# Kernel tuning notes

Measured on AMD Instinct MI355X. Metric: run time of the kernel, lower is better.

## Reference

```python
import jax, jax.numpy as jnp
import numpy as np

C_IN = 256
C_KEY = 128
C_VAL = 256


def setup_inputs() -> dict:
    key = jax.random.key(0)
    ks = jax.random.split(key, 10)
    B, H, W = 8, 64, 64
    s_in = 1.0 / np.sqrt(C_IN)
    s_val = 1.0 / np.sqrt(C_VAL)
    return {
        "x": jax.random.normal(ks[0], (B, C_IN, H, W), jnp.float32),
        "Wk": jax.random.uniform(ks[1], (C_KEY, C_IN), jnp.float32, -s_in, s_in),
        "bk": jax.random.uniform(ks[2], (C_KEY,), jnp.float32, -s_in, s_in),
        "Wq": jax.random.uniform(ks[3], (C_KEY, C_IN), jnp.float32, -s_in, s_in),
        "bq": jax.random.uniform(ks[4], (C_KEY,), jnp.float32, -s_in, s_in),
        "Wv": jax.random.uniform(ks[5], (C_VAL, C_IN), jnp.float32, -s_in, s_in),
        "bv": jax.random.uniform(ks[6], (C_VAL,), jnp.float32, -s_in, s_in),
        "Wr": jax.random.uniform(ks[7], (C_IN, C_VAL), jnp.float32, -s_val, s_val),
        "br": jax.random.uniform(ks[8], (C_IN,), jnp.float32, -s_val, s_val),
        "gamma": jnp.zeros((1,), jnp.float32) + 0.5,  # nonzero so attention path is exercised
    }


def reference(x, Wk, bk, Wq, bq, Wv, bv, Wr, br, gamma):
    B, C, H, W = x.shape
    N = H * W
    xf = x.reshape(B, C, N)  # [B, C, N]
    # 1x1 convs == per-pixel linear projections
    k = jnp.einsum('kc,bcn->bkn', Wk, xf) + bk[None, :, None]   # [B, Ck, N]
    q = jnp.einsum('kc,bcn->bkn', Wq, xf) + bq[None, :, None]   # [B, Ck, N]
    v = jnp.einsum('vc,bcn->bvn', Wv, xf) + bv[None, :, None]   # [B, Cv, N]
    # attention = q^T k, softmax over keys (no scaling, per original)
    att = jnp.einsum('bkq,bkn->bqn', q, k)                      # [B, N, N]
    att = jax.nn.softmax(att, axis=-1)
    out = jnp.einsum('bvn,bqn->bvq', v, att)                    # [B, Cv, N]
    out = jnp.einsum('cv,bvn->bcn', Wr, out) + br[None, :, None]
    out = out.reshape(B, C, H, W)
    return gamma * out + x
```

## Files before the change

### kernel.cpp

```cpp
#include <hip/hip_runtime.h>
#include <hip/hip_bf16.h>
#include <stdint.h>

#define NPIX 4096

typedef __attribute__((ext_vector_type(8))) short bf16x8;
typedef __attribute__((ext_vector_type(16))) float f32x16;
typedef __attribute__((ext_vector_type(4))) unsigned int uint4v;

__device__ __forceinline__ unsigned short bfb(float f) {
  __hip_bfloat16 h = __float2bfloat16(f);
  return __builtin_bit_cast(unsigned short, h);
}
__device__ __forceinline__ unsigned pack2(float a, float b) {
  return (unsigned)bfb(a) | ((unsigned)bfb(b) << 16);
}
__device__ __forceinline__ f32x16 mfma32(bf16x8 a, bf16x8 b, f32x16 c) {
  return __builtin_amdgcn_mfma_f32_32x32x16_bf16(a, b, c, 0, 0, 0);
}

__global__ void k_cvt(const float* __restrict__ Wq, const float* __restrict__ Wk,
                      const float* __restrict__ Wv, const float* __restrict__ Wr,
                      unsigned short* __restrict__ wqk, unsigned short* __restrict__ wv,
                      unsigned short* __restrict__ wr) {
  int i = blockIdx.x * 256 + threadIdx.x;
  wqk[i] = bfb(i < 32768 ? Wq[i] : Wk[i - 32768]);
  wv[i]  = bfb(Wv[i]);
  wr[i]  = bfb(Wr[i]);
}

__launch_bounds__(256, 2)
__global__ void k_qkv(const float* __restrict__ x,
                      const unsigned short* __restrict__ wqk,
                      const unsigned short* __restrict__ wv,
                      const float* __restrict__ bq, const float* __restrict__ bk,
                      const float* __restrict__ bv,
                      unsigned short* __restrict__ qT, unsigned short* __restrict__ kT,
                      unsigned short* __restrict__ vV) {
  __shared__ __align__(16) unsigned short xT[64 * 256];
  const int b = blockIdx.x & 7;
  const int n0 = (blockIdx.x >> 3) * 64;
  const int t = threadIdx.x;
  const float* xb = x + (size_t)b * 256 * NPIX;
  #pragma unroll
  for (int p = 0; p < 16; ++p) {
    int c = (t >> 4) + p * 16;
    int nq = (t & 15) * 4;
    float4 f = *reinterpret_cast<const float4*>(xb + (size_t)c * NPIX + n0 + nq);
    float vals[4] = {f.x, f.y, f.z, f.w};
    #pragma unroll
    for (int j = 0; j < 4; ++j) {
      int n = nq + j;
      int byteoff = n * 512 + ((c * 2) ^ ((n & 7) << 4));
      xT[byteoff >> 1] = bfb(vals[j]);
    }
  }
  __syncthreads();
  const int lane = t & 63, w = t >> 6, l31 = lane & 31, hi = lane >> 5;
  f32x16 aq[2][2], av[2][2];
  #pragma unroll
  for (int a0 = 0; a0 < 2; ++a0)
    #pragma unroll
    for (int a1 = 0; a1 < 2; ++a1)
      #pragma unroll
      for (int i = 0; i < 16; ++i) { aq[a0][a1][i] = 0.f; av[a0][a1][i] = 0.f; }
  #pragma unroll
  for (int s = 0; s < 16; ++s) {
    bf16x8 xa[2];
    #pragma unroll
    for (int nt = 0; nt < 2; ++nt) {
      int n = nt * 32 + l31;
      int byteoff = n * 512 + (((s * 32 + hi * 16)) ^ ((n & 7) << 4));
      xa[nt] = *reinterpret_cast<const bf16x8*>(reinterpret_cast<const char*>(xT) + byteoff);
    }
    #pragma unroll
    for (int oc2 = 0; oc2 < 2; ++oc2) {
      int oc = w * 64 + oc2 * 32 + l31;
      bf16x8 wq = *reinterpret_cast<const bf16x8*>(wqk + oc * 256 + s * 16 + hi * 8);
      bf16x8 wvf = *reinterpret_cast<const bf16x8*>(wv + oc * 256 + s * 16 + hi * 8);
      #pragma unroll
      for (int nt = 0; nt < 2; ++nt) {
        aq[oc2][nt] = mfma32(xa[nt], wq, aq[oc2][nt]);
        av[oc2][nt] = mfma32(wvf, xa[nt], av[oc2][nt]);
      }
    }
  }
  #pragma unroll
  for (int oc2 = 0; oc2 < 2; ++oc2) {
    int oc = w * 64 + oc2 * 32 + l31;
    float bias = (oc < 128) ? bq[oc] : bk[oc - 128];
    unsigned short* dst = (oc < 128) ? (qT + (size_t)b * NPIX * 128 + oc)
                                     : (kT + (size_t)b * NPIX * 128 + (oc - 128));
    #pragma unroll
    for (int nt = 0; nt < 2; ++nt)
      #pragma unroll
      for (int r = 0; r < 16; ++r) {
        int n = n0 + nt * 32 + (r & 3) + 8 * (r >> 2) + 4 * hi;
        dst[(size_t)n * 128] = bfb(aq[oc2][nt][r] + bias);
      }
  }
  unsigned short* vb = vV + (size_t)b * 256 * NPIX;
  #pragma unroll
  for (int vc2 = 0; vc2 < 2; ++vc2)
    #pragma unroll
    for (int nt = 0; nt < 2; ++nt)
      #pragma unroll
      for (int r = 0; r < 16; ++r) {
        int vc = w * 64 + vc2 * 32 + (r & 3) + 8 * (r >> 2) + 4 * hi;
        int n = n0 + nt * 32 + l31;
        vb[(size_t)vc * NPIX + n] = bfb(av[vc2][nt][r] + bv[vc]);
      }
}

__launch_bounds__(256, 1)
__global__ void k_attn(const unsigned short* __restrict__ qT,
                       const unsigned short* __restrict__ kT,
                       const unsigned short* __restrict__ vV,
                       unsigned short* __restrict__ oT) {
  __shared__ __align__(16) char smem[98304];
  const int b = blockIdx.x & 7;
  const int qt = blockIdx.x >> 3;
  const int t = threadIdx.x, lane = t & 63, l31 = lane & 31, hi = lane >> 5;
  const int sw = t >> 6;
  const int qp = qt * 128 + sw * 32 + l31;
  const unsigned short* qTb = qT + (size_t)b * NPIX * 128;
  const char* kTb = (const char*)(kT + (size_t)b * NPIX * 128);
  const char* vb  = (const char*)(vV + (size_t)b * 256 * NPIX);

  int kGl[4], kLds[4];
  #pragma unroll
  for (int i = 0; i < 4; ++i) {
    int row = sw * 16 + i * 4 + (lane >> 4);
    int c2 = (lane & 15) * 16;
    kGl[i]  = row * 256 + c2;
    kLds[i] = row * 256 + (c2 ^ ((row & 15) << 4));
  }
  int vGl[8], vLds[8];
  #pragma unroll
  for (int i = 0; i < 8; ++i) {
    int vc = sw * 64 + i * 8 + (lane >> 3);
    int c2 = (lane & 7) * 16;
    vGl[i]  = vc * 8192 + c2;
    vLds[i] = (vc >> 1) * 256 + (((vc & 1) * 128 + c2) ^ (((vc >> 1) & 15) << 4));
  }
  int kRowBase[2], kRowSwz[2];
  #pragma unroll
  for (int rt = 0; rt < 2; ++rt) {
    int row = rt * 32 + l31;
    kRowBase[rt] = row * 256;
    kRowSwz[rt]  = (row & 15) << 4;
  }
  int vBase[8], vSwz[8], vHalf;
  #pragma unroll
  for (int vt = 0; vt < 8; ++vt) {
    int vc = vt * 32 + l31;
    vBase[vt] = (vc >> 1) * 256;
    vSwz[vt]  = ((vc >> 1) & 15) << 4;
  }
  vHalf = (l31 & 1) * 128;

  bf16x8 qf[8];
  #pragma unroll
  for (int s = 0; s < 8; ++s)
    qf[s] = *reinterpret_cast<const bf16x8*>(qTb + (size_t)qp * 128 + s * 16 + hi * 8);
  f32x16 O[8];
  #pragma unroll
  for (int vt = 0; vt < 8; ++vt)
    #pragma unroll
    for (int i = 0; i < 16; ++i) O[vt][i] = 0.f;
  float m_run = -3.0e38f, l_run = 0.0f;

  uint4v stK[4], stV[8];
  #pragma unroll
  for (int i = 0; i < 4; ++i) stK[i] = *reinterpret_cast<const uint4v*>(kTb + kGl[i]);
  #pragma unroll
  for (int i = 0; i < 8; ++i) stV[i] = *reinterpret_cast<const uint4v*>(vb + vGl[i]);
  #pragma unroll
  for (int i = 0; i < 4; ++i) *reinterpret_cast<uint4v*>(smem + kLds[i]) = stK[i];
  #pragma unroll
  for (int i = 0; i < 8; ++i) *reinterpret_cast<uint4v*>(smem + 16384 + vLds[i]) = stV[i];
  __syncthreads();

  for (int kt = 0; kt < 64; ++kt) {
    const int cur = kt & 1;
    char* Kl = smem + cur * 49152;
    char* Vl = smem + cur * 49152 + 16384;
    if (kt < 63) {
      const char* kg = kTb + (size_t)(kt + 1) * 16384;
      const char* vg = vb + (size_t)(kt + 1) * 128;
      #pragma unroll
      for (int i = 0; i < 4; ++i) stK[i] = *reinterpret_cast<const uint4v*>(kg + kGl[i]);
      #pragma unroll
      for (int i = 0; i < 8; ++i) stV[i] = *reinterpret_cast<const uint4v*>(vg + vGl[i]);
      __builtin_amdgcn_sched_barrier(0);
    }
    #pragma unroll
    for (int rt = 0; rt < 2; ++rt) {
      f32x16 S;
      #pragma unroll
      for (int i = 0; i < 16; ++i) S[i] = 0.f;
      __builtin_amdgcn_s_setprio(1);
      #pragma unroll
      for (int s = 0; s < 8; ++s) {
        bf16x8 ka = *reinterpret_cast<const bf16x8*>(
            Kl + kRowBase[rt] + ((s * 32 + hi * 16) ^ kRowSwz[rt]));
        S = mfma32(ka, qf[s], S);
      }
      __builtin_amdgcn_s_setprio(0);
      float mx = fmaxf(fmaxf(fmaxf(S[0], S[1]), fmaxf(S[2], S[3])),
                       fmaxf(fmaxf(S[4], S[5]), fmaxf(S[6], S[7])));
      mx = fmaxf(mx, fmaxf(fmaxf(fmaxf(S[8], S[9]), fmaxf(S[10], S[11])),
                           fmaxf(fmaxf(S[12], S[13]), fmaxf(S[14], S[15]))));
      mx = fmaxf(mx, __shfl_xor(mx, 32));
      if (__any(mx > m_run + 8.0f)) {
        float mn = fmaxf(m_run, mx);
        float al = __expf(m_run - mn);
        l_run *= al;
        #pragma unroll
        for (int vt = 0; vt < 8; ++vt)
          #pragma unroll
          for (int i = 0; i < 16; ++i) O[vt][i] *= al;
        m_run = mn;
      }
      float sum = 0.f;
      #pragma unroll
      for (int i = 0; i < 16; ++i) { S[i] = __expf(S[i] - m_run); sum += S[i]; }
      sum += __shfl_xor(sum, 32);
      l_run += sum;
      unsigned wd[8];
      #pragma unroll
      for (int i = 0; i < 8; ++i) wd[i] = pack2(S[2 * i], S[2 * i + 1]);
      #pragma unroll
      for (int pr = 0; pr < 4; ++pr) {
        int ia = (pr & 1) + (pr >> 1) * 4;
        int ib = ia + 2;
        unsigned xs = (unsigned)__shfl_xor((int)wd[ia], 32);
        unsigned ys = (unsigned)__shfl_xor((int)wd[ib], 32);
        unsigned na = hi ? ys : wd[ia];
        unsigned nb = hi ? wd[ib] : xs;
        wd[ia] = na; wd[ib] = nb;
      }
      bf16x8 pf[2];
      { uint4v u; u.x = wd[0]; u.y = wd[1]; u.z = wd[2]; u.w = wd[3];
        pf[0] = __builtin_bit_cast(bf16x8, u); }
      { uint4v u; u.x = wd[4]; u.y = wd[5]; u.z = wd[6]; u.w = wd[7];
        pf[1] = __builtin_bit_cast(bf16x8, u); }
      __builtin_amdgcn_s_setprio(1);
      #pragma unroll
      for (int sl = 0; sl < 2; ++sl) {
        int ks = rt * 2 + sl;
        #pragma unroll
        for (int vt = 0; vt < 8; ++vt) {
          bf16x8 va = *reinterpret_cast<const bf16x8*>(
              Vl + vBase[vt] + ((vHalf + ks * 32 + hi * 16) ^ vSwz[vt]));
          O[vt] = mfma32(va, pf[sl], O[vt]);
        }
      }
      __builtin_amdgcn_s_setprio(0);
    }
    __syncthreads();
    if (kt < 63) {
      char* Kn = smem + (cur ^ 1) * 49152;
      char* Vn = smem + (cur ^ 1) * 49152 + 16384;
      #pragma unroll
      for (int i = 0; i < 4; ++i) *reinterpret_cast<uint4v*>(Kn + kLds[i]) = stK[i];
      #pragma unroll
      for (int i = 0; i < 8; ++i) *reinterpret_cast<uint4v*>(Vn + vLds[i]) = stV[i];
    }
    __syncthreads();
  }
  float rl = 1.0f / l_run;
  unsigned short* oTb = oT + (size_t)b * NPIX * 256;
  #pragma unroll
  for (int vt = 0; vt < 8; ++vt)
    #pragma unroll
    for (int i = 0; i < 16; i += 2) {
      int vc = vt * 32 + (i & 3) + 8 * (i >> 2) + 4 * hi;
      unsigned pk = pack2(O[vt][i] * rl, O[vt][i + 1] * rl);
      *reinterpret_cast<unsigned*>(oTb + (size_t)qp * 256 + vc) = pk;
    }
}

__launch_bounds__(256, 2)
__global__ void k_out(const unsigned short* __restrict__ oT,
                      const unsigned short* __restrict__ wr,
                      const float* __restrict__ br, const float* __restrict__ gamma,
                      const float* __restrict__ x, float* __restrict__ out) {
  const int b = blockIdx.x & 7;
  const int n0 = (blockIdx.x >> 3) * 64;
  const int t = threadIdx.x, w = t >> 6, lane = t & 63, l31 = lane & 31, hi = lane >> 5;
  const unsigned short* oTb = oT + (size_t)b * NPIX * 256;
  f32x16 acc[2][2];
  #pragma unroll
  for (int a0 = 0; a0 < 2; ++a0)
    #pragma unroll
    for (int a1 = 0; a1 < 2; ++a1)
      #pragma unroll
      for (int i = 0; i < 16; ++i) acc[a0][a1][i] = 0.f;
  #pragma unroll
  for (int s = 0; s < 16; ++s) {
    bf16x8 ofr[2], wfr[2];
    #pragma unroll
    for (int nt = 0; nt < 2; ++nt) {
      int n = n0 + nt * 32 + l31;
      ofr[nt] = *reinterpret_cast<const bf16x8*>(oTb + (size_t)n * 256 + s * 16 + hi * 8);
    }
    #pragma unroll
    for (int c2 = 0; c2 < 2; ++c2) {
      int c = w * 64 + c2 * 32 + l31;
      wfr[c2] = *reinterpret_cast<const bf16x8*>(wr + c * 256 + s * 16 + hi * 8);
    }
    #pragma unroll
    for (int c2 = 0; c2 < 2; ++c2)
      #pragma unroll
      for (int nt = 0; nt < 2; ++nt)
        acc[c2][nt] = mfma32(wfr[c2], ofr[nt], acc[c2][nt]);
  }
  float g = gamma[0];
  #pragma unroll
  for (int c2 = 0; c2 < 2; ++c2)
    #pragma unroll
    for (int nt = 0; nt < 2; ++nt)
      #pragma unroll
      for (int r = 0; r < 16; ++r) {
        int c = w * 64 + c2 * 32 + (r & 3) + 8 * (r >> 2) + 4 * hi;
        int n = n0 + nt * 32 + l31;
        size_t idx = (size_t)b * 256 * NPIX + (size_t)c * NPIX + n;
        out[idx] = g * (acc[c2][nt][r] + br[c]) + x[idx];
      }
}

extern "C" void kernel_launch(void* const* d_in, const int* in_sizes, int n_in,
                              void* d_out, int out_size, void* d_ws, size_t ws_size,
                              hipStream_t stream) {
  const float* x     = (const float*)d_in[0];
  const float* Wk    = (const float*)d_in[1];
  const float* bk    = (const float*)d_in[2];
  const float* Wq    = (const float*)d_in[3];
  const float* bq    = (const float*)d_in[4];
  const float* Wv    = (const float*)d_in[5];
  const float* bv    = (const float*)d_in[6];
  const float* Wr    = (const float*)d_in[7];
  const float* br    = (const float*)d_in[8];
  const float* gamma = (const float*)d_in[9];

  const size_t OFF_QT  = 0;
  const size_t OFF_KT  = 8388608;
  const size_t OFF_V   = 16777216;
  const size_t OFF_OT  = 33554432;
  const size_t OFF_WQK = 50331648;
  const size_t OFF_WV  = 50462720;
  const size_t OFF_WR  = 50593792;
  const size_t NEED    = 50724864;
  if (ws_size < NEED) return;

  char* ws = (char*)d_ws;
  unsigned short* qT  = (unsigned short*)(ws + OFF_QT);
  unsigned short* kT  = (unsigned short*)(ws + OFF_KT);
  unsigned short* vV  = (unsigned short*)(ws + OFF_V);
  unsigned short* oT  = (unsigned short*)(ws + OFF_OT);
  unsigned short* wqk = (unsigned short*)(ws + OFF_WQK);
  unsigned short* wvb = (unsigned short*)(ws + OFF_WV);
  unsigned short* wrb = (unsigned short*)(ws + OFF_WR);

  k_cvt<<<256, 256, 0, stream>>>(Wq, Wk, Wv, Wr, wqk, wvb, wrb);
  k_qkv<<<512, 256, 0, stream>>>(x, wqk, wvb, bq, bk, bv, qT, kT, vV);
  k_attn<<<256, 256, 0, stream>>>(qT, kT, vV, oT);
  k_out<<<512, 256, 0, stream>>>(oT, wrb, br, gamma, x, (float*)d_out);
}
```

Baseline: 264.3 us.

## Split attention over two key halves and merge partials with log-sum-exp

The attention kernel can now split the key range in two, launching twice as many blocks. Each block writes a normalized partial output plus its log-sum-exp, and the output projection kernel merges the two partials with softmax weights before the MFMA matmul. The register-staged double buffer is replaced by a single 48KB shared-memory tile so two blocks fit per CU. This aims to fill the device better than 256 one-per-CU blocks. The cost is extra partial-output traffic, merge arithmetic in k_out, and loss of the prefetch overlap. The split path only runs when the workspace is large enough.

```diff
diff --git a/kernel.cpp b/kernel.cpp
--- a/kernel.cpp
+++ b/kernel.cpp
@@ -14,6 +14,9 @@
 }
 __device__ __forceinline__ unsigned pack2(float a, float b) {
   return (unsigned)bfb(a) | ((unsigned)bfb(b) << 16);
+}
+__device__ __forceinline__ float bs(short v) {
+  return __builtin_bit_cast(float, (unsigned)(unsigned short)v << 16);
 }
 __device__ __forceinline__ f32x16 mfma32(bf16x8 a, bf16x8 b, f32x16 c) {
   return __builtin_amdgcn_mfma_f32_32x32x16_bf16(a, b, c, 0, 0, 0);
@@ -112,14 +115,20 @@
       }
 }
 
-__launch_bounds__(256, 1)
+__launch_bounds__(256, 2)
 __global__ void k_attn(const unsigned short* __restrict__ qT,
                        const unsigned short* __restrict__ kT,
                        const unsigned short* __restrict__ vV,
-                       unsigned short* __restrict__ oT) {
-  __shared__ __align__(16) char smem[98304];
+                       unsigned short* __restrict__ o0,
+                       unsigned short* __restrict__ o1,
+                       float* __restrict__ lse, int split) {
+  __shared__ __align__(16) char smem[49152];
   const int b = blockIdx.x & 7;
-  const int qt = blockIdx.x >> 3;
+  const int rest = blockIdx.x >> 3;
+  const int qt = rest >> split;
+  const int h = rest & split;
+  const int nkt = 64 >> split;
+  const int kt0 = h * nkt;
   const int t = threadIdx.x, lane = t & 63, l31 = lane & 31, hi = lane >> 5;
   const int sw = t >> 6;
   const int qp = qt * 128 + sw * 32 + l31;
@@ -150,14 +159,14 @@
     kRowBase[rt] = row * 256;
     kRowSwz[rt]  = (row & 15) << 4;
   }
-  int vBase[8], vSwz[8], vHalf;
+  int vBase[8], vSwz[8];
   #pragma unroll
   for (int vt = 0; vt < 8; ++vt) {
     int vc = vt * 32 + l31;
     vBase[vt] = (vc >> 1) * 256;
     vSwz[vt]  = ((vc >> 1) & 15) << 4;
   }
-  vHalf = (l31 & 1) * 128;
+  const int vHalf = (l31 & 1) * 128;
 
   bf16x8 qf[8];
   #pragma unroll
@@ -170,30 +179,22 @@
     for (int i = 0; i < 16; ++i) O[vt][i] = 0.f;
   float m_run = -3.0e38f, l_run = 0.0f;
 
-  uint4v stK[4], stV[8];
-  #pragma unroll
-  for (int i = 0; i < 4; ++i) stK[i] = *reinterpret_cast<const uint4v*>(kTb + kGl[i]);
-  #pragma unroll
-  for (int i = 0; i < 8; ++i) stV[i] = *reinterpret_cast<const uint4v*>(vb + vGl[i]);
-  #pragma unroll
-  for (int i = 0; i < 4; ++i) *reinterpret_cast<uint4v*>(smem + kLds[i]) = stK[i];
-  #pragma unroll
-  for (int i = 0; i < 8; ++i) *reinterpret_cast<uint4v*>(smem + 16384 + vLds[i]) = stV[i];
-  __syncthreads();
-
-  for (int kt = 0; kt < 64; ++kt) {
-    const int cur = kt & 1;
-    char* Kl = smem + cur * 49152;
-    char* Vl = smem + cur * 49152 + 16384;
-    if (kt < 63) {
-      const char* kg = kTb + (size_t)(kt + 1) * 16384;
-      const char* vg = vb + (size_t)(kt + 1) * 128;
-      #pragma unroll
-      for (int i = 0; i < 4; ++i) stK[i] = *reinterpret_cast<const uint4v*>(kg + kGl[i]);
-      #pragma unroll
-      for (int i = 0; i < 8; ++i) stV[i] = *reinterpret_cast<const uint4v*>(vg + vGl[i]);
-      __builtin_amdgcn_sched_barrier(0);
-    }
+  for (int kt = kt0; kt < kt0 + nkt; ++kt) {
+    const char* kg = kTb + (size_t)kt * 16384;
+    const char* vg = vb + (size_t)kt * 128;
+    char* Kl = smem;
+    char* Vl = smem + 16384;
+    #pragma unroll
+    for (int i = 0; i < 4; ++i) {
+      uint4v d = *reinterpret_cast<const uint4v*>(kg + kGl[i]);
+      *reinterpret_cast<uint4v*>(Kl + kLds[i]) = d;
+    }
+    #pragma unroll
+    for (int i = 0; i < 8; ++i) {
+      uint4v d = *reinterpret_cast<const uint4v*>(vg + vGl[i]);
+      *reinterpret_cast<uint4v*>(Vl + vLds[i]) = d;
+    }
+    __syncthreads();
     #pragma unroll
     for (int rt = 0; rt < 2; ++rt) {
       f32x16 S;
@@ -259,37 +260,45 @@
       __builtin_amdgcn_s_setprio(0);
     }
     __syncthreads();
-    if (kt < 63) {
-      char* Kn = smem + (cur ^ 1) * 49152;
-      char* Vn = smem + (cur ^ 1) * 49152 + 16384;
-      #pragma unroll
-      for (int i = 0; i < 4; ++i) *reinterpret_cast<uint4v*>(Kn + kLds[i]) = stK[i];
-      #pragma unroll
-      for (int i = 0; i < 8; ++i) *reinterpret_cast<uint4v*>(Vn + vLds[i]) = stV[i];
-    }
-    __syncthreads();
   }
   float rl = 1.0f / l_run;
-  unsigned short* oTb = oT + (size_t)b * NPIX * 256;
+  unsigned short* oPtr = (h ? o1 : o0) + (size_t)b * NPIX * 256;
   #pragma unroll
   for (int vt = 0; vt < 8; ++vt)
     #pragma unroll
     for (int i = 0; i < 16; i += 2) {
       int vc = vt * 32 + (i & 3) + 8 * (i >> 2) + 4 * hi;
       unsigned pk = pack2(O[vt][i] * rl, O[vt][i + 1] * rl);
-      *reinterpret_cast<unsigned*>(oTb + (size_t)qp * 256 + vc) = pk;
-    }
+      *reinterpret_cast<unsigned*>(oPtr + (size_t)qp * 256 + vc) = pk;
+    }
+  lse[h * 32768 + b * 4096 + qp] = m_run + __logf(l_run);
 }
 
 __launch_bounds__(256, 2)
-__global__ void k_out(const unsigned short* __restrict__ oT,
+__global__ void k_out(const unsigned short* __restrict__ o0,
+                      const unsigned short* __restrict__ o1,
+                      const float* __restrict__ lse0, const float* __restrict__ lse1,
                       const unsigned short* __restrict__ wr,
                       const float* __restrict__ br, const float* __restrict__ gamma,
                       const float* __restrict__ x, float* __restrict__ out) {
   const int b = blockIdx.x & 7;
   const int n0 = (blockIdx.x >> 3) * 64;
   const int t = threadIdx.x, w = t >> 6, lane = t & 63, l31 = lane & 31, hi = lane >> 5;
-  const unsigned short* oTb = oT + (size_t)b * NPIX * 256;
+  const unsigned short* o0b = o0 + (size_t)b * NPIX * 256;
+  const unsigned short* o1b = o1 + (size_t)b * NPIX * 256;
+  float w0f[2], w1f[2];
+  int nrow[2];
+  #pragma unroll
+  for (int nt = 0; nt < 2; ++nt) {
+    int n = n0 + nt * 32 + l31;
+    nrow[nt] = n;
+    float f0 = lse0[b * 4096 + n], f1 = lse1[b * 4096 + n];
+    float M = fmaxf(f0, f1);
+    float e0 = __expf(f0 - M), e1 = __expf(f1 - M);
+    float inv = 1.0f / (e0 + e1);
+    w0f[nt] = e0 * inv;
+    w1f[nt] = e1 * inv;
+  }
   f32x16 acc[2][2];
   #pragma unroll
   for (int a0 = 0; a0 < 2; ++a0)
@@ -302,8 +311,18 @@
     bf16x8 ofr[2], wfr[2];
     #pragma unroll
     for (int nt = 0; nt < 2; ++nt) {
-      int n = n0 + nt * 32 + l31;
-      ofr[nt] = *reinterpret_cast<const bf16x8*>(oTb + (size_t)n * 256 + s * 16 + hi * 8);
+      size_t off = (size_t)nrow[nt] * 256 + s * 16 + hi * 8;
+      bf16x8 a0 = *reinterpret_cast<const bf16x8*>(o0b + off);
+      bf16x8 a1 = *reinterpret_cast<const bf16x8*>(o1b + off);
+      unsigned u[4];
+      #pragma unroll
+      for (int p = 0; p < 4; ++p) {
+        float m0 = w0f[nt] * bs(a0[2 * p])     + w1f[nt] * bs(a1[2 * p]);
+        float m1 = w0f[nt] * bs(a0[2 * p + 1]) + w1f[nt] * bs(a1[2 * p + 1]);
+        u[p] = pack2(m0, m1);
+      }
+      uint4v uv; uv.x = u[0]; uv.y = u[1]; uv.z = u[2]; uv.w = u[3];
+      ofr[nt] = __builtin_bit_cast(bf16x8, uv);
     }
     #pragma unroll
     for (int c2 = 0; c2 < 2; ++c2) {
@@ -344,27 +363,34 @@
   const float* br    = (const float*)d_in[8];
   const float* gamma = (const float*)d_in[9];
 
-  const size_t OFF_QT  = 0;
-  const size_t OFF_KT  = 8388608;
-  const size_t OFF_V   = 16777216;
-  const size_t OFF_OT  = 33554432;
-  const size_t OFF_WQK = 50331648;
-  const size_t OFF_WV  = 50462720;
-  const size_t OFF_WR  = 50593792;
-  const size_t NEED    = 50724864;
-  if (ws_size < NEED) return;
+  const size_t OFF_QT = 0;
+  const size_t OFF_KT = 8388608;
+  const size_t OFF_V  = 16777216;
+  const size_t OFF_O0 = 33554432;
+  const size_t OFF_O1 = 50331648;
+  const size_t NEED_SPLIT = 67502080;
+  const size_t NEED_BASE  = 50724864;
+  if (ws_size < NEED_BASE) return;
+  const int split = (ws_size >= NEED_SPLIT) ? 1 : 0;
+  const size_t OFF_WQK = split ? 67108864 : 50331648;
+  const size_t OFF_WV  = OFF_WQK + 131072;
+  const size_t OFF_WR  = OFF_WQK + 262144;
+  const size_t OFF_LSE = OFF_WQK;
 
   char* ws = (char*)d_ws;
   unsigned short* qT  = (unsigned short*)(ws + OFF_QT);
   unsigned short* kT  = (unsigned short*)(ws + OFF_KT);
   unsigned short* vV  = (unsigned short*)(ws + OFF_V);
-  unsigned short* oT  = (unsigned short*)(ws + OFF_OT);
+  unsigned short* o0  = (unsigned short*)(ws + OFF_O0);
+  unsigned short* o1  = split ? (unsigned short*)(ws + OFF_O1) : o0;
   unsigned short* wqk = (unsigned short*)(ws + OFF_WQK);
   unsigned short* wvb = (unsigned short*)(ws + OFF_WV);
   unsigned short* wrb = (unsigned short*)(ws + OFF_WR);
+  float* lse = (float*)(ws + OFF_LSE);
+  float* lse1 = lse + (split ? 32768 : 0);
 
   k_cvt<<<256, 256, 0, stream>>>(Wq, Wk, Wv, Wr, wqk, wvb, wrb);
   k_qkv<<<512, 256, 0, stream>>>(x, wqk, wvb, bq, bk, bv, qT, kT, vV);
-  k_attn<<<256, 256, 0, stream>>>(qT, kT, vV, oT);
-  k_out<<<512, 256, 0, stream>>>(oT, wrb, br, gamma, x, (float*)d_out);
-}
+  k_attn<<<split ? 512 : 256, 256, 0, stream>>>(qT, kT, vV, o0, o1, lse, split);
+  k_out<<<512, 256, 0, stream>>>(o0, o1, lse, lse1, wrb, br, gamma, x, (float*)d_out);
+}
```

After: 258.2 us. -2.3%, faster.

## Stage K/V tiles with direct global-to-LDS loads, dropping register staging

Applied to the files above, without the earlier changes.

Replaces the register-staged K/V prefetch (global load into VGPRs, then ds_write after a barrier) with global_load_lds async copies straight into the next LDS buffer. The swizzle is moved from the destination to the source address because the LDS destination is fixed per wave. One of the two per-iteration barriers is removed. This frees staging registers and removes the LDS write pass, but depends on the vmcnt wait before the barrier being placed correctly to avoid reading incomplete tiles.

```diff
diff --git a/kernel.cpp b/kernel.cpp
--- a/kernel.cpp
+++ b/kernel.cpp
@@ -7,6 +7,8 @@
 typedef __attribute__((ext_vector_type(8))) short bf16x8;
 typedef __attribute__((ext_vector_type(16))) float f32x16;
 typedef __attribute__((ext_vector_type(4))) unsigned int uint4v;
+typedef __attribute__((address_space(1))) unsigned int gu32;
+typedef __attribute__((address_space(3))) unsigned int lu32;
 
 __device__ __forceinline__ unsigned short bfb(float f) {
   __hip_bfloat16 h = __float2bfloat16(f);
@@ -127,21 +129,24 @@
   const char* kTb = (const char*)(kT + (size_t)b * NPIX * 128);
   const char* vb  = (const char*)(vV + (size_t)b * 256 * NPIX);
 
-  int kGl[4], kLds[4];
+  int kSrc[4], kDst[4];
   #pragma unroll
   for (int i = 0; i < 4; ++i) {
-    int row = sw * 16 + i * 4 + (lane >> 4);
+    int c = sw * 4 + i;
+    int row = c * 4 + (lane >> 4);
     int c2 = (lane & 15) * 16;
-    kGl[i]  = row * 256 + c2;
-    kLds[i] = row * 256 + (c2 ^ ((row & 15) << 4));
-  }
-  int vGl[8], vLds[8];
+    kSrc[i] = row * 256 + (c2 ^ ((row & 15) << 4));
+    kDst[i] = c * 1024;
+  }
+  int vSrc[8], vDst[8];
   #pragma unroll
   for (int i = 0; i < 8; ++i) {
-    int vc = sw * 64 + i * 8 + (lane >> 3);
-    int c2 = (lane & 7) * 16;
-    vGl[i]  = vc * 8192 + c2;
-    vLds[i] = (vc >> 1) * 256 + (((vc & 1) * 128 + c2) ^ (((vc >> 1) & 15) << 4));
+    int c = sw * 8 + i;
+    int pr = c * 4 + (lane >> 4);
+    int z = ((lane & 15) * 16) ^ ((pr & 15) << 4);
+    int vc = pr * 2 + (z >> 7);
+    vSrc[i] = vc * 8192 + (z & 127);
+    vDst[i] = 16384 + c * 1024;
   }
   int kRowBase[2], kRowSwz[2];
   #pragma unroll
@@ -150,14 +155,14 @@
     kRowBase[rt] = row * 256;
     kRowSwz[rt]  = (row & 15) << 4;
   }
-  int vBase[8], vSwz[8], vHalf;
+  int vBase[8], vSwz[8];
   #pragma unroll
   for (int vt = 0; vt < 8; ++vt) {
     int vc = vt * 32 + l31;
     vBase[vt] = (vc >> 1) * 256;
     vSwz[vt]  = ((vc >> 1) & 15) << 4;
   }
-  vHalf = (l31 & 1) * 128;
+  const int vHalf = (l31 & 1) * 128;
 
   bf16x8 qf[8];
   #pragma unroll
@@ -170,30 +175,26 @@
     for (int i = 0; i < 16; ++i) O[vt][i] = 0.f;
   float m_run = -3.0e38f, l_run = 0.0f;
 
-  uint4v stK[4], stV[8];
-  #pragma unroll
-  for (int i = 0; i < 4; ++i) stK[i] = *reinterpret_cast<const uint4v*>(kTb + kGl[i]);
-  #pragma unroll
-  for (int i = 0; i < 8; ++i) stV[i] = *reinterpret_cast<const uint4v*>(vb + vGl[i]);
-  #pragma unroll
-  for (int i = 0; i < 4; ++i) *reinterpret_cast<uint4v*>(smem + kLds[i]) = stK[i];
-  #pragma unroll
-  for (int i = 0; i < 8; ++i) *reinterpret_cast<uint4v*>(smem + 16384 + vLds[i]) = stV[i];
+  auto STAGE = [&](char* buf, int kt) {
+    const char* kg = kTb + (size_t)kt * 16384;
+    const char* vg = vb + (size_t)kt * 128;
+    #pragma unroll
+    for (int i = 0; i < 4; ++i)
+      __builtin_amdgcn_global_load_lds((gu32*)(kg + kSrc[i]),
+                                       (lu32*)(buf + kDst[i]), 16, 0, 0);
+    #pragma unroll
+    for (int i = 0; i < 8; ++i)
+      __builtin_amdgcn_global_load_lds((gu32*)(vg + vSrc[i]),
+                                       (lu32*)(buf + vDst[i]), 16, 0, 0);
+  };
+
+  STAGE(smem, 0);
   __syncthreads();
 
   for (int kt = 0; kt < 64; ++kt) {
-    const int cur = kt & 1;
-    char* Kl = smem + cur * 49152;
-    char* Vl = smem + cur * 49152 + 16384;
-    if (kt < 63) {
-      const char* kg = kTb + (size_t)(kt + 1) * 16384;
-      const char* vg = vb + (size_t)(kt + 1) * 128;
-      #pragma unroll
-      for (int i = 0; i < 4; ++i) stK[i] = *reinterpret_cast<const uint4v*>(kg + kGl[i]);
-      #pragma unroll
-      for (int i = 0; i < 8; ++i) stV[i] = *reinterpret_cast<const uint4v*>(vg + vGl[i]);
-      __builtin_amdgcn_sched_barrier(0);
-    }
+    char* Kl = smem + (kt & 1) * 49152;
+    char* Vl = Kl + 16384;
+    if (kt < 63) STAGE(smem + ((kt + 1) & 1) * 49152, kt + 1);
     #pragma unroll
     for (int rt = 0; rt < 2; ++rt) {
       f32x16 S;
@@ -259,15 +260,6 @@
       __builtin_amdgcn_s_setprio(0);
     }
     __syncthreads();
-    if (kt < 63) {
-      char* Kn = smem + (cur ^ 1) * 49152;
-      char* Vn = smem + (cur ^ 1) * 49152 + 16384;
-      #pragma unroll
-      for (int i = 0; i < 4; ++i) *reinterpret_cast<uint4v*>(Kn + kLds[i]) = stK[i];
-      #pragma unroll
-      for (int i = 0; i < 8; ++i) *reinterpret_cast<uint4v*>(Vn + vLds[i]) = stV[i];
-    }
-    __syncthreads();
   }
   float rl = 1.0f / l_run;
   unsigned short* oTb = oT + (size_t)b * NPIX * 256;
```

After: 237.4 us. 10.2% less time.
